# Kernel tuning notes

Hardware: AMD Instinct MI355X
Metric: run time of the kernel (lower is better)

The kernel has to match this reference:

```python
import jax, jax.numpy as jnp
import numpy as np

N, E, D, H, OUT, L, G = 50000, 800000, 128, 128, 128, 5, 512
EMB = L * H  # 640
BN_EPS = 1e-5


def setup_inputs() -> dict:
    key = jax.random.key(0)
    ks = jax.random.split(key, 24)
    s_h = 1.0 / np.sqrt(H)
    s_e = 1.0 / np.sqrt(EMB)
    inp = {
        'x': jax.random.normal(ks[0], (N, D), jnp.float32),
        'edge_index': jax.random.randint(ks[1], (2, E), 0, N, jnp.int32),
        'batch': jnp.sort(jax.random.randint(ks[2], (N,), 0, G, jnp.int32)),
        # per-layer GINConv MLP: Linear(D/H->H), BN(H), ReLU, Linear(H->H). D==H so stackable.
        'conv_W1': jax.random.normal(ks[3], (L, H, H), jnp.float32) * s_h,
        'conv_b1': jnp.zeros((L, H), jnp.float32),
        'conv_g1': jnp.ones((L, H), jnp.float32),
        'conv_be1': jnp.zeros((L, H), jnp.float32),
        'conv_W2': jax.random.normal(ks[4], (L, H, H), jnp.float32) * s_h,
        'conv_b2': jnp.zeros((L, H), jnp.float32),
        'eps': jnp.zeros((L,), jnp.float32),  # train_eps=True, init 0.0
        # outer BatchNorm per layer
        'bn_g': jnp.ones((L, H), jnp.float32),
        'bn_b': jnp.zeros((L, H), jnp.float32),
        # per-layer prediction heads Linear(H -> OUT)
        'pred_W': jax.random.normal(ks[5], (L, H, OUT), jnp.float32) * s_h,
        'pred_b': jnp.zeros((L, OUT), jnp.float32),
        # global_d FF(EMB): 3 stacked Linear(EMB,EMB) + shortcut
        'gW': jax.random.normal(ks[6], (3, EMB, EMB), jnp.float32) * s_e,
        'gb': jnp.zeros((3, EMB), jnp.float32),
        'gsW': jax.random.normal(ks[7], (EMB, EMB), jnp.float32) * s_e,
        'gsb': jnp.zeros((EMB,), jnp.float32),
        # local_d FF(EMB)
        'lW': jax.random.normal(ks[8], (3, EMB, EMB), jnp.float32) * s_e,
        'lb': jnp.zeros((3, EMB), jnp.float32),
        'lsW': jax.random.normal(ks[9], (EMB, EMB), jnp.float32) * s_e,
        'lsb': jnp.zeros((EMB,), jnp.float32),
    }
    return inp


def _bn(h, g, b):
    # BatchNorm1d, training mode: batch stats over node dim (biased var)
    m = jnp.mean(h, axis=0)
    v = jnp.var(h, axis=0)
    return g * (h - m) * jax.lax.rsqrt(v + BN_EPS) + b


def _ff(x, W, b, Ws, bs):
    h = x
    for i in range(3):
        h = jax.nn.relu(h @ W[i] + b[i])
    return h + x @ Ws + bs


def reference(x, edge_index, batch, conv_W1, conv_b1, conv_g1, conv_be1,
              conv_W2, conv_b2, eps, bn_g, bn_b, pred_W, pred_b,
              gW, gb, gsW, gsb, lW, lb, lsW, lsb):
    src, dst = edge_index[0], edge_index[1]
    h = x
    xs = []
    for i in range(L):
        # GINConv: (1+eps)*x_i + sum_{j->i} x_j, then MLP
        agg = jax.ops.segment_sum(h[src], dst, num_segments=N)
        h = (1.0 + eps[i]) * h + agg
        h = _bn(h @ conv_W1[i] + conv_b1[i], conv_g1[i], conv_be1[i])
        h = jax.nn.relu(h)
        h = h @ conv_W2[i] + conv_b2[i]
        h = jax.nn.relu(_bn(h, bn_g[i], bn_b[i]))
        xs.append(h)
    # per-layer graph sum-pool + prediction head (dropout in eval = identity)
    xpool = [jax.ops.segment_sum(xs[i], batch, num_segments=G) @ pred_W[i] + pred_b[i]
             for i in range(L)]
    xcat = jnp.concatenate(xpool, axis=1)            # [G, L*OUT]
    graph_embedding = _ff(xcat, gW, gb, gsW, gsb)     # [G, EMB]
    node_embedding = _ff(jnp.concatenate(xs, axis=1), lW, lb, lsW, lsb)  # [N, EMB]
    return (graph_embedding, node_embedding, xcat)
```

## Files before the change

### kernel.cpp

```cpp
#include <hip/hip_runtime.h>

constexpr int H    = 128;
constexpr int LNUM = 5;
constexpr int NG   = 512;
constexpr int EMB  = 640;
constexpr float BN_EPS = 1e-5f;

typedef __attribute__((ext_vector_type(8))) short bf16x8;
typedef __attribute__((ext_vector_type(4))) float f32x4;

__device__ inline unsigned short f2bf(float f){
  unsigned u = __builtin_bit_cast(unsigned, f);
  u += 0x7FFF + ((u >> 16) & 1);
  return (unsigned short)(u >> 16);
}
__device__ inline float bf2f(unsigned short h){
  unsigned u = ((unsigned)h) << 16;
  return __builtin_bit_cast(float, u);
}

__device__ inline int xcd_swz(int bid, int nwg){
  int q = nwg >> 3, r = nwg & 7;
  int xcd = bid & 7, idx = bid >> 3;
  return (xcd < r ? xcd*(q+1) : r*(q+1) + (xcd-r)*q) + idx;
}

__global__ void k_zerof(float* p, int n){
  int i = blockIdx.x*256 + threadIdx.x;
  if (i < n) p[i] = 0.f;
}
__global__ void k_zeroi(int* p, int n){
  int i = blockIdx.x*256 + threadIdx.x;
  if (i < n) p[i] = 0;
}

__global__ void k_hist(const int* __restrict__ dst, int E, int* deg){
  int e = blockIdx.x*256 + threadIdx.x;
  if (e < E) atomicAdd(&deg[dst[e]], 1);
}

__global__ __launch_bounds__(1024) void k_scan(int* degcur, int* __restrict__ rowptr, int n){
  __shared__ int wsum[16];
  __shared__ int carry;
  int tid = threadIdx.x, wid = tid >> 6, lane = tid & 63;
  if (tid == 0){ carry = 0; rowptr[0] = 0; }
  __syncthreads();
  for (int base = 0; base < n; base += 1024){
    int v = (base + tid < n) ? degcur[base + tid] : 0;
    int s = v;
#pragma unroll
    for (int off = 1; off < 64; off <<= 1){
      int t = __shfl_up(s, off);
      if (lane >= off) s += t;
    }
    if (lane == 63) wsum[wid] = s;
    __syncthreads();
    if (wid == 0 && lane < 16){
      int wv = wsum[lane];
#pragma unroll
      for (int off = 1; off < 16; off <<= 1){
        int t = __shfl_up(wv, off);
        if (lane >= off) wv += t;
      }
      wsum[lane] = wv;
    }
    __syncthreads();
    int incl = s + (wid ? wsum[wid-1] : 0) + carry;
    if (base + tid < n){ rowptr[base + tid + 1] = incl; degcur[base + tid] = incl - v; }
    __syncthreads();
    if (tid == 0) carry += wsum[15];
    __syncthreads();
  }
}

__global__ void k_scatter(const int* __restrict__ src, const int* __restrict__ dst,
                          int E, int* cursor, int* __restrict__ colsrc){
  int e = blockIdx.x*256 + threadIdx.x;
  if (e < E){
    int d = dst[e];
    int pos = atomicAdd(&cursor[d], 1);
    colsrc[pos] = src[e];
  }
}

__global__ void k_gstart(const int* __restrict__ batch, int N, int* __restrict__ gstart){
  int g = blockIdx.x*256 + threadIdx.x;
  if (g <= NG){
    int lo = 0, hi = N;
    while (lo < hi){
      int mid = (lo + hi) >> 1;
      if (batch[mid] < g) lo = mid + 1; else hi = mid;
    }
    gstart[g] = lo;
  }
}

__global__ void k_castT(const float* __restrict__ W, unsigned short* __restrict__ Wt,
                        int K, int Nn, int ldt, int koff){
  __shared__ float sh[32][33];
  const size_t in_off  = (size_t)blockIdx.z * K * Nn;
  const size_t out_off = (size_t)blockIdx.z * Nn * ldt;
  int n0 = blockIdx.x*32, k0 = blockIdx.y*32;
  int tx = threadIdx.x, ty = threadIdx.y;
  for (int r = ty; r < 32; r += 8)
    sh[r][tx] = W[in_off + (size_t)(k0 + r)*Nn + n0 + tx];
  __syncthreads();
  for (int r = ty; r < 32; r += 8)
    Wt[out_off + (size_t)(n0 + r)*ldt + koff + k0 + tx] = f2bf(sh[tx][r]);
}

__global__ void k_bias2(const float* __restrict__ a, const float* __restrict__ b,
                        float* __restrict__ o){
  int i = threadIdx.x;
  o[i] = a[i] + b[i];
}

template<bool IN_BF16>
__global__ __launch_bounds__(256) void k_agg(const void* __restrict__ hin_, int ldh,
                                             const int* __restrict__ rowptr,
                                             const int* __restrict__ colsrc,
                                             const float* __restrict__ epsp,
                                             unsigned short* __restrict__ outp, int nN){
  int node = blockIdx.x*4 + (threadIdx.x >> 6);
  if (node >= nN) return;
  int lane = threadIdx.x & 63;
  float a0, a1;
  if (IN_BF16){
    unsigned u = ((const unsigned*)hin_)[((size_t)node*ldh >> 1) + lane];
    a0 = bf2f((unsigned short)u); a1 = bf2f((unsigned short)(u >> 16));
  } else {
    float2 f = ((const float2*)hin_)[((size_t)node*ldh >> 1) + lane];
    a0 = f.x; a1 = f.y;
  }
  float ep = 1.0f + *epsp;
  a0 *= ep; a1 *= ep;
  int e = rowptr[node], e1 = rowptr[node+1];
  const int ld2 = ldh >> 1;
  for (; e + 4 <= e1; e += 4){
    int s0 = colsrc[e], s1 = colsrc[e+1], s2 = colsrc[e+2], s3 = colsrc[e+3];
    if (IN_BF16){
      unsigned u0 = ((const unsigned*)hin_)[(size_t)s0*ld2 + lane];
      unsigned u1 = ((const unsigned*)hin_)[(size_t)s1*ld2 + lane];
      unsigned u2 = ((const unsigned*)hin_)[(size_t)s2*ld2 + lane];
      unsigned u3 = ((const unsigned*)hin_)[(size_t)s3*ld2 + lane];
      a0 += bf2f((unsigned short)u0) + bf2f((unsigned short)u1)
          + bf2f((unsigned short)u2) + bf2f((unsigned short)u3);
      a1 += bf2f((unsigned short)(u0 >> 16)) + bf2f((unsigned short)(u1 >> 16))
          + bf2f((unsigned short)(u2 >> 16)) + bf2f((unsigned short)(u3 >> 16));
    } else {
      float2 f0 = ((const float2*)hin_)[(size_t)s0*ld2 + lane];
      float2 f1 = ((const float2*)hin_)[(size_t)s1*ld2 + lane];
      float2 f2 = ((const float2*)hin_)[(size_t)s2*ld2 + lane];
      float2 f3 = ((const float2*)hin_)[(size_t)s3*ld2 + lane];
      a0 += f0.x + f1.x + f2.x + f3.x;
      a1 += f0.y + f1.y + f2.y + f3.y;
    }
  }
  for (; e < e1; ++e){
    int s = colsrc[e];
    if (IN_BF16){
      unsigned u = ((const unsigned*)hin_)[(size_t)s*ld2 + lane];
      a0 += bf2f((unsigned short)u); a1 += bf2f((unsigned short)(u >> 16));
    } else {
      float2 f = ((const float2*)hin_)[(size_t)s*ld2 + lane];
      a0 += f.x; a1 += f.y;
    }
  }
  ((unsigned*)outp)[((size_t)node*H >> 1) + lane] =
      (unsigned)f2bf(a0) | ((unsigned)f2bf(a1) << 16);
}

__global__ void k_bnfin(float* sums, float* sumsq,
                        const float* __restrict__ g, const float* __restrict__ b,
                        float* __restrict__ scale, float* __restrict__ shift, float invn){
  int c = threadIdx.x;
  float m = sums[c]*invn;
  float v = sumsq[c]*invn - m*m;
  float inv = rsqrtf(v + BN_EPS);
  float sc = g[c]*inv;
  scale[c] = sc;
  shift[c] = b[c] - m*sc;
  sums[c] = 0.f; sumsq[c] = 0.f;
}

__global__ __launch_bounds__(256) void k_bnapply(const unsigned short* __restrict__ U,
                                                 const float* __restrict__ scale,
                                                 const float* __restrict__ shift,
                                                 unsigned short* __restrict__ out,
                                                 int ldo, int n){
  int i = blockIdx.x*256 + threadIdx.x;
  int total = n * (H/4);
  if (i < total){
    int r = i >> 5;
    int c4 = (i & 31) << 2;
    uint2 up = *(const uint2*)(U + (size_t)r*H + c4);
    float4 sc = *(const float4*)(scale + c4);
    float4 sf = *(const float4*)(shift + c4);
    float a = fmaxf(fmaf(sc.x, bf2f((unsigned short)up.x),        sf.x), 0.f);
    float b = fmaxf(fmaf(sc.y, bf2f((unsigned short)(up.x>>16)),  sf.y), 0.f);
    float c = fmaxf(fmaf(sc.z, bf2f((unsigned short)up.y),        sf.z), 0.f);
    float d = fmaxf(fmaf(sc.w, bf2f((unsigned short)(up.y>>16)),  sf.w), 0.f);
    uint2 o;
    o.x = (unsigned)f2bf(a) | ((unsigned)f2bf(b) << 16);
    o.y = (unsigned)f2bf(c) | ((unsigned)f2bf(d) << 16);
    *(uint2*)(out + (size_t)r*ldo + c4) = o;
  }
}

__global__ __launch_bounds__(320) void k_pool(const unsigned short* __restrict__ xall,
                                              const int* __restrict__ gstart,
                                              float* __restrict__ pooled){
  int g = blockIdx.x;
  int t = threadIdx.x;
  int n0 = gstart[g], n1 = gstart[g+1];
  float a0 = 0.f, a1 = 0.f;
  for (int n = n0; n < n1; ++n){
    unsigned u = ((const unsigned*)xall)[(size_t)n*(EMB/2) + t];
    a0 += bf2f((unsigned short)u); a1 += bf2f((unsigned short)(u >> 16));
  }
  *(float2*)(pooled + (size_t)g*EMB + 2*t) = make_float2(a0, a1);
}

__global__ __launch_bounds__(128) void k_pred(const float* __restrict__ pooled,
                                              const float* __restrict__ W,
                                              const float* __restrict__ b,
                                              float* __restrict__ xcat){
  int g = blockIdx.x, l = blockIdx.y, o = threadIdx.x;
  __shared__ float sh[128];
  sh[o] = pooled[(size_t)g*EMB + l*H + o];
  __syncthreads();
  const float* Wl = W + (size_t)l*H*H;
  float acc = b[l*H + o];
  for (int k = 0; k < H; ++k) acc = fmaf(sh[k], Wl[k*H + o], acc);
  xcat[(size_t)g*EMB + l*H + o] = acc;
}

template<bool RELU, bool OUT_BF16, bool DUAL>
__global__ __launch_bounds__(512) void k_mm(
    const unsigned short* __restrict__ A, int lda,
    const unsigned short* __restrict__ A2,
    const unsigned short* __restrict__ Bt, int ldb,
    const float* __restrict__ bias,
    void* __restrict__ Cv, int ldc,
    int M, int K)
{
  __shared__ union LdsU {
    unsigned short stage[2][2][128*64];
    unsigned short sc16[128*136];
    float          sc32[128*132];
  } u;
  const int tid  = threadIdx.x;
  const int lane = tid & 63;
  const int w    = tid >> 6;
  const int wr   = w >> 2, wc = w & 3;

  const int nwg = gridDim.x * gridDim.y;
  const int bid = blockIdx.y * gridDim.x + blockIdx.x;
  const int wg  = xcd_swz(bid, nwg);
  const int col0 = (wg % gridDim.x) * 128;
  const int row0 = (wg / gridDim.x) * 128;
  const int KA   = DUAL ? (K >> 1) : K;

  const unsigned short *sA[2], *sA2[2], *sB[2];
  int dOff[2];
#pragma unroll
  for (int j = 0; j < 2; ++j){
    int d = w*2048 + j*1024 + lane*16;
    int m = d >> 7;
    int inner = (d & 127) ^ ((m & 7) << 4);
    int gm = row0 + m; if (gm > M-1) gm = M-1;
    sA[j]  = A  + (size_t)gm*lda + (inner >> 1);
    if (DUAL) sA2[j] = A2 + (size_t)gm*lda + (inner >> 1);
    sB[j]  = Bt + (size_t)(col0 + m)*ldb + (inner >> 1);
    dOff[j] = w*2048 + j*1024;
  }

  f32x4 acc[4][2];
#pragma unroll
  for (int i = 0; i < 4; ++i)
#pragma unroll
    for (int j = 0; j < 2; ++j)
      acc[i][j] = (f32x4){0.f, 0.f, 0.f, 0.f};

  auto STAGE = [&](int buf, int kt){
    int k0 = kt*64;
    int ka = k0;
    bool second = DUAL && (k0 >= KA);
    if (second) ka = k0 - KA;
#pragma unroll
    for (int j = 0; j < 2; ++j){
      const unsigned short* srcA = second ? (sA2[j] + ka) : (sA[j] + ka);
      __builtin_amdgcn_global_load_lds(
          (const __attribute__((address_space(1))) void*)srcA,
          (__attribute__((address_space(3))) void*)((char*)&u.stage[buf][0][0] + dOff[j]),
          16, 0, 0);
    }
#pragma unroll
    for (int j = 0; j < 2; ++j)
      __builtin_amdgcn_global_load_lds(
          (const __attribute__((address_space(1))) void*)(sB[j] + k0),
          (__attribute__((address_space(3))) void*)((char*)&u.stage[buf][1][0] + dOff[j]),
          16, 0, 0);
  };

  auto COMPUTE = [&](int buf){
    const char* Ab = (const char*)&u.stage[buf][0][0];
    const char* Bb = (const char*)&u.stage[buf][1][0];
#pragma unroll
    for (int kk = 0; kk < 2; ++kk){
      const int kb = kk*64 + ((lane >> 4) << 4);
      bf16x8 af[4], bfr[2];
#pragma unroll
      for (int i = 0; i < 4; ++i){
        int row = wr*64 + i*16 + (lane & 15);
        int ab  = (row*128 + kb) ^ ((row & 7) << 4);
        af[i] = *(const bf16x8*)(Ab + ab);
      }
#pragma unroll
      for (int j = 0; j < 2; ++j){
        int col = wc*32 + j*16 + (lane & 15);
        int bb  = (col*128 + kb) ^ ((col & 7) << 4);
        bfr[j] = *(const bf16x8*)(Bb + bb);
      }
#pragma unroll
      for (int i = 0; i < 4; ++i)
#pragma unroll
        for (int j = 0; j < 2; ++j)
          acc[i][j] = __builtin_amdgcn_mfma_f32_16x16x32_bf16(af[i], bfr[j], acc[i][j], 0, 0, 0);
    }
  };

  const int NT = K / 64;
  STAGE(0, 0);
  STAGE(1, 1);
  asm volatile("s_waitcnt vmcnt(4)" ::: "memory");
  __syncthreads();

  int cur = 0;
  for (int t = 0; t < NT; ++t){
    COMPUTE(cur);
    if (t == NT-1) break;
    __syncthreads();
    if (t + 2 < NT){
      STAGE(cur, t + 2);
      asm volatile("s_waitcnt vmcnt(4)" ::: "memory");
    } else {
      asm volatile("s_waitcnt vmcnt(0)" ::: "memory");
    }
    __syncthreads();
    cur ^= 1;
  }

  __syncthreads();
  if (OUT_BF16){
#pragma unroll
    for (int j = 0; j < 2; ++j){
      int cl = wc*32 + j*16 + (lane & 15);
      float bs = bias[col0 + cl];
#pragma unroll
      for (int i = 0; i < 4; ++i){
        int rb = wr*64 + i*16 + ((lane >> 4) << 2);
#pragma unroll
        for (int r = 0; r < 4; ++r){
          float v = acc[i][j][r] + bs;
          if (RELU) v = fmaxf(v, 0.f);
          u.sc16[(rb + r)*136 + cl] = f2bf(v);
        }
      }
    }
    __syncthreads();
    unsigned short* Cb = (unsigned short*)Cv;
    for (int idx = tid; idx < 128*16; idx += 512){
      int rr = idx >> 4, seg = idx & 15;
      int grow = row0 + rr;
      if (grow < M){
        uint4 vv = *(const uint4*)&u.sc16[rr*136 + seg*8];
        *(uint4*)(Cb + (size_t)grow*ldc + col0 + seg*8) = vv;
      }
    }
  } else {
#pragma unroll
    for (int j = 0; j < 2; ++j){
      int cl = wc*32 + j*16 + (lane & 15);
      float bs = bias[col0 + cl];
#pragma unroll
      for (int i = 0; i < 4; ++i){
        int rb = wr*64 + i*16 + ((lane >> 4) << 2);
#pragma unroll
        for (int r = 0; r < 4; ++r){
          float v = acc[i][j][r] + bs;
          if (RELU) v = fmaxf(v, 0.f);
          u.sc32[(rb + r)*132 + cl] = v;
        }
      }
    }
    __syncthreads();
    float* Cf = (float*)Cv;
    for (int idx = tid; idx < 128*32; idx += 512){
      int rr = idx >> 5, seg = idx & 31;
      int grow = row0 + rr;
      if (grow < M){
        float4 vv = *(const float4*)&u.sc32[rr*132 + seg*4];
        *(float4*)(Cf + (size_t)grow*ldc + col0 + seg*4) = vv;
      }
    }
  }
}

template<bool PRO_BN, bool STATS>
__global__ __launch_bounds__(512) void k_mmc(
    const unsigned short* __restrict__ A,
    const unsigned short* __restrict__ Bt,
    const float* __restrict__ bias,
    const float* __restrict__ kscale, const float* __restrict__ kshift,
    unsigned short* __restrict__ C, int ldc,
    float* sums, float* sumsq,
    int M)
{
  __shared__ unsigned short shm[2*128*128];
  unsigned short* As = shm;
  unsigned short* Bs = shm + 128*128;
  const int tid  = threadIdx.x;
  const int lane = tid & 63;
  const int w    = tid >> 6;
  const int wr   = w >> 2, wc = w & 3;

  const int wg   = xcd_swz(blockIdx.x, gridDim.x);
  const int row0 = wg * 128;

#pragma unroll
  for (int j = 0; j < 4; ++j){
    int d = w*4096 + j*1024 + lane*16;
    int m = d >> 8;
    int inner = (d & 255) ^ ((m & 15) << 4);
    int gm = row0 + m; if (gm > M-1) gm = M-1;
    __builtin_amdgcn_global_load_lds(
        (const __attribute__((address_space(1))) void*)(A + (size_t)gm*H + (inner >> 1)),
        (__attribute__((address_space(3))) void*)((char*)As + w*4096 + j*1024),
        16, 0, 0);
    __builtin_amdgcn_global_load_lds(
        (const __attribute__((address_space(1))) void*)(Bt + (size_t)m*H + (inner >> 1)),
        (__attribute__((address_space(3))) void*)((char*)Bs + w*4096 + j*1024),
        16, 0, 0);
  }
  asm volatile("s_waitcnt vmcnt(0)" ::: "memory");
  __syncthreads();

  f32x4 acc[4][2];
#pragma unroll
  for (int i = 0; i < 4; ++i)
#pragma unroll
    for (int j = 0; j < 2; ++j)
      acc[i][j] = (f32x4){0.f, 0.f, 0.f, 0.f};

#pragma unroll
  for (int kk = 0; kk < 4; ++kk){
    const int kb = kk*64 + ((lane >> 4) << 4);
    bf16x8 af[4], bfr[2];
#pragma unroll
    for (int i = 0; i < 4; ++i){
      int row = wr*64 + i*16 + (lane & 15);
      int ab  = (row*256 + kb) ^ ((row & 15) << 4);
      af[i] = *(const bf16x8*)((const char*)As + ab);
    }
#pragma unroll
    for (int j = 0; j < 2; ++j){
      int col = wc*32 + j*16 + (lane & 15);
      int bb  = (col*256 + kb) ^ ((col & 15) << 4);
      bfr[j] = *(const bf16x8*)((const char*)Bs + bb);
    }
    if (PRO_BN){
      int k8 = kk*32 + ((lane >> 4) << 3);
      float4 s0 = *(const float4*)(kscale + k8), s1 = *(const float4*)(kscale + k8 + 4);
      float4 f0 = *(const float4*)(kshift + k8), f1 = *(const float4*)(kshift + k8 + 4);
      float sc[8] = {s0.x,s0.y,s0.z,s0.w,s1.x,s1.y,s1.z,s1.w};
      float sf[8] = {f0.x,f0.y,f0.z,f0.w,f1.x,f1.y,f1.z,f1.w};
#pragma unroll
      for (int i = 0; i < 4; ++i){
        bf16x8 a = af[i], o;
#pragma unroll
        for (int jj = 0; jj < 8; ++jj){
          float v = fmaxf(fmaf(sc[jj], bf2f((unsigned short)a[jj]), sf[jj]), 0.f);
          o[jj] = (short)f2bf(v);
        }
        af[i] = o;
      }
    }
#pragma unroll
    for (int i = 0; i < 4; ++i)
#pragma unroll
      for (int j = 0; j < 2; ++j)
        acc[i][j] = __builtin_amdgcn_mfma_f32_16x16x32_bf16(af[i], bfr[j], acc[i][j], 0, 0, 0);
  }

  if (STATS){
#pragma unroll
    for (int j = 0; j < 2; ++j){
      int col = wc*32 + j*16 + (lane & 15);
      float bs = bias[col];
      float s = 0.f, q = 0.f;
#pragma unroll
      for (int i = 0; i < 4; ++i){
        int rb = row0 + wr*64 + i*16 + ((lane >> 4) << 2);
#pragma unroll
        for (int r = 0; r < 4; ++r){
          if (rb + r < M){
            float v = acc[i][j][r] + bs;
            s += v; q += v*v;
          }
        }
      }
      s += __shfl_xor(s, 16); q += __shfl_xor(q, 16);
      s += __shfl_xor(s, 32); q += __shfl_xor(q, 32);
      if (lane < 16){
        atomicAdd(&sums[col], s);
        atomicAdd(&sumsq[col], q);
      }
    }
  }

  __syncthreads();
#pragma unroll
  for (int j = 0; j < 2; ++j){
    int cl = wc*32 + j*16 + (lane & 15);
    float bs = bias[cl];
#pragma unroll
    for (int i = 0; i < 4; ++i){
      int rb = wr*64 + i*16 + ((lane >> 4) << 2);
#pragma unroll
      for (int r = 0; r < 4; ++r)
        shm[(rb + r)*136 + cl] = f2bf(acc[i][j][r] + bs);
    }
  }
  __syncthreads();
  for (int idx = tid; idx < 128*16; idx += 512){
    int rr = idx >> 4, seg = idx & 15;
    int grow = row0 + rr;
    if (grow < M){
      uint4 vv = *(const uint4*)&shm[rr*136 + seg*8];
      *(uint4*)(C + (size_t)grow*ldc + seg*8) = vv;
    }
  }
}

template<bool RELU, bool ADD_D>
__global__ __launch_bounds__(256) void k_gemm64(
    const float* __restrict__ A, int lda,
    const float* __restrict__ B, int ldb,
    const float* __restrict__ bias,
    const float* D, int ldd,
    float* C, int ldc,
    int M, int N, int K)
{
  __shared__ float As[32][68];
  __shared__ float Bs[32][64];
  const int tid  = threadIdx.x;
  const int tx   = tid & 15;
  const int ty   = tid >> 4;
  const int row0 = blockIdx.x * 64;
  const int col0 = blockIdx.y * 64;
  const int am = tid >> 3;
  const int ak = (tid & 7) << 2;
  const int bk = tid >> 4;
  const int bn = (tid & 15) << 2;
  float acc[4][4] = {};

  for (int k0 = 0; k0 < K; k0 += 32){
#pragma unroll
    for (int h = 0; h < 2; ++h){
      int m  = am + h*32;
      int gr = row0 + m;
      float4 v = make_float4(0.f, 0.f, 0.f, 0.f);
      if (gr < M) v = *(const float4*)(A + (size_t)gr*lda + k0 + ak);
      As[ak+0][m]=v.x; As[ak+1][m]=v.y; As[ak+2][m]=v.z; As[ak+3][m]=v.w;
    }
#pragma unroll
    for (int h = 0; h < 2; ++h){
      int kk = bk + h*16;
      *(float4*)(&Bs[kk][bn]) = *(const float4*)(B + (size_t)(k0+kk)*ldb + col0 + bn);
    }
    __syncthreads();
#pragma unroll 8
    for (int k = 0; k < 32; ++k){
      float4 a = *(const float4*)(&As[k][ty<<2]);
      float4 b = *(const float4*)(&Bs[k][tx<<2]);
      float av[4] = {a.x,a.y,a.z,a.w};
      float bv[4] = {b.x,b.y,b.z,b.w};
#pragma unroll
      for (int i = 0; i < 4; ++i)
#pragma unroll
        for (int j = 0; j < 4; ++j)
          acc[i][j] = fmaf(av[i], bv[j], acc[i][j]);
    }
    __syncthreads();
  }

  const int col = col0 + (tx<<2);
  float4 bv = *(const float4*)(bias + col);
#pragma unroll
  for (int i = 0; i < 4; ++i){
    int row = row0 + (ty<<2) + i;
    if (row < M){
      float r[4] = {acc[i][0]+bv.x, acc[i][1]+bv.y, acc[i][2]+bv.z, acc[i][3]+bv.w};
      if (RELU){
#pragma unroll
        for (int j = 0; j < 4; ++j) r[j] = fmaxf(r[j], 0.f);
      }
      if (ADD_D){
        float4 d = *(const float4*)(D + (size_t)row*ldd + col);
        r[0]+=d.x; r[1]+=d.y; r[2]+=d.z; r[3]+=d.w;
      }
      *(float4*)(C + (size_t)row*ldc + col) = make_float4(r[0],r[1],r[2],r[3]);
    }
  }
}

extern "C" void kernel_launch(void* const* d_in, const int* in_sizes, int n_in,
                              void* d_out, int out_size, void* d_ws, size_t ws_size,
                              hipStream_t stream) {
  const float* x        = (const float*)d_in[0];
  const int*   ei       = (const int*)d_in[1];
  const int*   batch    = (const int*)d_in[2];
  const float* conv_W1  = (const float*)d_in[3];
  const float* conv_b1  = (const float*)d_in[4];
  const float* conv_g1  = (const float*)d_in[5];
  const float* conv_be1 = (const float*)d_in[6];
  const float* conv_W2  = (const float*)d_in[7];
  const float* conv_b2  = (const float*)d_in[8];
  const float* epsv     = (const float*)d_in[9];
  const float* bn_g     = (const float*)d_in[10];
  const float* bn_b     = (const float*)d_in[11];
  const float* pred_W   = (const float*)d_in[12];
  const float* pred_b   = (const float*)d_in[13];
  const float* gW       = (const float*)d_in[14];
  const float* gb       = (const float*)d_in[15];
  const float* gsW      = (const float*)d_in[16];
  const float* gsb      = (const float*)d_in[17];
  const float* lW       = (const float*)d_in[18];
  const float* lb       = (const float*)d_in[19];
  const float* lsW      = (const float*)d_in[20];
  const float* lsb      = (const float*)d_in[21];

  const int N = in_sizes[0] / H;
  const int E = in_sizes[1] / 2;
  const int* srcI = ei;
  const int* dstI = ei + E;

  float* out = (float*)d_out;
  float* GE = out;
  float* NE = out + (size_t)NG*EMB;
  float* XC = NE + (size_t)N*EMB;

  unsigned short* xall = (unsigned short*)d_ws;
  unsigned short* h1   = xall + (size_t)N*EMB;
  unsigned short* h2   = h1 + (size_t)N*EMB;
  unsigned short* hpre = h1;
  unsigned short* ub   = h1 + (size_t)N*H;
  unsigned short* tb   = h1 + (size_t)2*N*H;

  float* pooled  = (float*)(h2 + (size_t)N*EMB);
  float* gtmp1   = pooled + (size_t)NG*EMB;
  float* gtmp2   = gtmp1 + (size_t)NG*EMB;
  float* sums    = gtmp2 + (size_t)NG*EMB;
  float* sumsq   = sums + 128;
  float* bnscale = sumsq + 128;
  float* bnshift = bnscale + 128;
  float* biasNE  = bnshift + 128;
  unsigned short* W1t   = (unsigned short*)(biasNE + EMB);
  unsigned short* W2t   = W1t + (size_t)LNUM*H*H;
  unsigned short* lWt01 = W2t + (size_t)LNUM*H*H;
  unsigned short* Wcat  = lWt01 + (size_t)2*EMB*EMB;
  int* rowptr = (int*)(Wcat + (size_t)2*EMB*EMB);
  int* cursor = rowptr + (N + 1);
  int* colsrc = cursor + N;
  int* gstart = colsrc + E;

  k_zerof<<<1, 256, 0, stream>>>(sums, 256);

  k_zeroi<<<(N+255)/256, 256, 0, stream>>>(cursor, N);
  k_hist<<<(E+255)/256, 256, 0, stream>>>(dstI, E, cursor);
  k_scan<<<1, 1024, 0, stream>>>(cursor, rowptr, N);
  k_scatter<<<(E+255)/256, 256, 0, stream>>>(srcI, dstI, E, cursor, colsrc);
  k_gstart<<<(NG+256)/256, 256, 0, stream>>>(batch, N, gstart);

  const dim3 tb32(32, 8);
  k_castT<<<dim3(H/32, H/32, LNUM), tb32, 0, stream>>>(conv_W1, W1t, H, H, H, 0);
  k_castT<<<dim3(H/32, H/32, LNUM), tb32, 0, stream>>>(conv_W2, W2t, H, H, H, 0);
  k_castT<<<dim3(EMB/32, EMB/32, 2), tb32, 0, stream>>>(lW, lWt01, EMB, EMB, EMB, 0);
  k_castT<<<dim3(EMB/32, EMB/32, 1), tb32, 0, stream>>>(lW + (size_t)2*EMB*EMB, Wcat,
                                                        EMB, EMB, 2*EMB, 0);
  k_castT<<<dim3(EMB/32, EMB/32, 1), tb32, 0, stream>>>(lsW, Wcat, EMB, EMB, 2*EMB, EMB);
  k_bias2<<<1, EMB, 0, stream>>>(lb + (size_t)2*EMB, lsb, biasNE);

  const float invn = 1.0f / (float)N;
  const int nrow = (N + 127)/128;

  for (int l = 0; l < LNUM; ++l){
    if (l == 0)
      k_agg<false><<<(N+3)/4, 256, 0, stream>>>(x, H, rowptr, colsrc, epsv, hpre, N);
    else
      k_agg<true><<<(N+3)/4, 256, 0, stream>>>(xall + (size_t)(l-1)*H, EMB, rowptr, colsrc,
                                               epsv + l, hpre, N);

    k_mmc<false,true><<<nrow, 512, 0, stream>>>(
        hpre, W1t + (size_t)l*H*H, conv_b1 + l*H, nullptr, nullptr,
        ub, H, sums, sumsq, N);
    k_bnfin<<<1, 128, 0, stream>>>(sums, sumsq, conv_g1 + l*H, conv_be1 + l*H,
                                   bnscale, bnshift, invn);
    k_mmc<true,true><<<nrow, 512, 0, stream>>>(
        ub, W2t + (size_t)l*H*H, conv_b2 + l*H, bnscale, bnshift,
        tb, H, sums, sumsq, N);
    k_bnfin<<<1, 128, 0, stream>>>(sums, sumsq, bn_g + l*H, bn_b + l*H,
                                   bnscale, bnshift, invn);
    k_bnapply<<<(N*32 + 255)/256, 256, 0, stream>>>(tb, bnscale, bnshift,
                                                    xall + (size_t)l*H, EMB, N);
  }

  k_pool<<<NG, 320, 0, stream>>>(xall, gstart, pooled);
  k_pred<<<dim3(NG, LNUM), 128, 0, stream>>>(pooled, pred_W, pred_b, XC);

  const dim3 gg((NG + 63)/64, EMB/64);
  k_gemm64<false,false><<<gg, 256, 0, stream>>>(XC, EMB, gsW, EMB, gsb,
                                                nullptr, 0, GE, EMB, NG, EMB, EMB);
  k_gemm64<true,false><<<gg, 256, 0, stream>>>(XC, EMB, gW, EMB, gb,
                                               nullptr, 0, gtmp1, EMB, NG, EMB, EMB);
  k_gemm64<true,false><<<gg, 256, 0, stream>>>(gtmp1, EMB, gW + (size_t)EMB*EMB, EMB, gb + EMB,
                                               nullptr, 0, gtmp2, EMB, NG, EMB, EMB);
  k_gemm64<true,true><<<gg, 256, 0, stream>>>(gtmp2, EMB, gW + (size_t)2*EMB*EMB, EMB, gb + 2*EMB,
                                              GE, EMB, GE, EMB, NG, EMB, EMB);

  const dim3 gn(EMB/128, nrow);
  k_mm<true,true,false><<<gn, 512, 0, stream>>>(
      xall, EMB, nullptr, lWt01, EMB, lb, h1, EMB, N, EMB);
  k_mm<true,true,false><<<gn, 512, 0, stream>>>(
      h1, EMB, nullptr, lWt01 + (size_t)EMB*EMB, EMB, lb + EMB, h2, EMB, N, EMB);
  k_mm<false,false,true><<<gn, 512, 0, stream>>>(
      h2, EMB, xall, Wcat, 2*EMB, biasNE, NE, EMB, N, 2*EMB);
}
```

Measured before the change: 1.181 ms.

## Enlarge node-FF GEMM tile to 256x128 with triple-buffered LDS staging

The k_mm GEMM used for the three node-embedding feed-forward layers now computes 256x128 output tiles per 512-thread block instead of 128x128. Each wave handles a 64x64 sub-tile with 16 MFMA accumulators, which raises arithmetic intensity per LDS load and halves how often B is re-read. The staging pipeline moves from two to three LDS buffers, issuing the next load before compute so there is one barrier per k-step instead of two. The fp32 epilogue writes its output in two halves to fit the shared-memory union. The cost is more LDS per block (144 KB for staging) and more accumulator registers, which lowers occupancy, and a coarser grid of about 196x5 blocks.

New measurement: 1.195 ms. No clear change (+1.2%).

```diff
diff --git a/kernel.cpp b/kernel.cpp
--- a/kernel.cpp
+++ b/kernel.cpp
@@ -245,87 +245,92 @@
     int M, int K)
 {
   __shared__ union LdsU {
-    unsigned short stage[2][2][128*64];
-    unsigned short sc16[128*136];
+    unsigned short stage[3][24576];
+    unsigned short sc16[256*136];
     float          sc32[128*132];
   } u;
   const int tid  = threadIdx.x;
   const int lane = tid & 63;
   const int w    = tid >> 6;
-  const int wr   = w >> 2, wc = w & 3;
+  const int wr   = w >> 1, wc = w & 1;
 
   const int nwg = gridDim.x * gridDim.y;
   const int bid = blockIdx.y * gridDim.x + blockIdx.x;
   const int wg  = xcd_swz(bid, nwg);
   const int col0 = (wg % gridDim.x) * 128;
-  const int row0 = (wg / gridDim.x) * 128;
+  const int row0 = (wg / gridDim.x) * 256;
   const int KA   = DUAL ? (K >> 1) : K;
 
-  const unsigned short *sA[2], *sA2[2], *sB[2];
-  int dOff[2];
+  const unsigned short *sA[4], *sA2[4], *sB[2];
+  int dA[4], dB[2];
+#pragma unroll
+  for (int j = 0; j < 4; ++j){
+    int d = w*4096 + j*1024 + lane*16;
+    int m = d >> 7;
+    int inner = (d & 127) ^ ((m & 7) << 4);
+    int gm = row0 + m; if (gm > M-1) gm = M-1;
+    sA[j] = A + (size_t)gm*lda + (inner >> 1);
+    if (DUAL) sA2[j] = A2 + (size_t)gm*lda + (inner >> 1);
+    dA[j] = w*4096 + j*1024;
+  }
 #pragma unroll
   for (int j = 0; j < 2; ++j){
     int d = w*2048 + j*1024 + lane*16;
     int m = d >> 7;
     int inner = (d & 127) ^ ((m & 7) << 4);
-    int gm = row0 + m; if (gm > M-1) gm = M-1;
-    sA[j]  = A  + (size_t)gm*lda + (inner >> 1);
-    if (DUAL) sA2[j] = A2 + (size_t)gm*lda + (inner >> 1);
-    sB[j]  = Bt + (size_t)(col0 + m)*ldb + (inner >> 1);
-    dOff[j] = w*2048 + j*1024;
-  }
-
-  f32x4 acc[4][2];
+    sB[j] = Bt + (size_t)(col0 + m)*ldb + (inner >> 1);
+    dB[j] = 32768 + w*2048 + j*1024;
+  }
+
+  f32x4 acc[4][4];
 #pragma unroll
   for (int i = 0; i < 4; ++i)
 #pragma unroll
-    for (int j = 0; j < 2; ++j)
+    for (int j = 0; j < 4; ++j)
       acc[i][j] = (f32x4){0.f, 0.f, 0.f, 0.f};
 
   auto STAGE = [&](int buf, int kt){
-    int k0 = kt*64;
-    int ka = k0;
+    int k0 = kt*64, ka = k0;
     bool second = DUAL && (k0 >= KA);
     if (second) ka = k0 - KA;
-#pragma unroll
-    for (int j = 0; j < 2; ++j){
-      const unsigned short* srcA = second ? (sA2[j] + ka) : (sA[j] + ka);
+    char* base = (char*)&u.stage[buf][0];
+#pragma unroll
+    for (int j = 0; j < 4; ++j){
+      const unsigned short* s = second ? (sA2[j] + ka) : (sA[j] + ka);
       __builtin_amdgcn_global_load_lds(
-          (const __attribute__((address_space(1))) void*)srcA,
-          (__attribute__((address_space(3))) void*)((char*)&u.stage[buf][0][0] + dOff[j]),
+          (const __attribute__((address_space(1))) void*)s,
+          (__attribute__((address_space(3))) void*)(base + dA[j]),
           16, 0, 0);
     }
 #pragma unroll
     for (int j = 0; j < 2; ++j)
       __builtin_amdgcn_global_load_lds(
           (const __attribute__((address_space(1))) void*)(sB[j] + k0),
-          (__attribute__((address_space(3))) void*)((char*)&u.stage[buf][1][0] + dOff[j]),
+          (__attribute__((address_space(3))) void*)(base + dB[j]),
           16, 0, 0);
   };
 
   auto COMPUTE = [&](int buf){
-    const char* Ab = (const char*)&u.stage[buf][0][0];
-    const char* Bb = (const char*)&u.stage[buf][1][0];
+    const char* Ab = (const char*)&u.stage[buf][0];
+    const char* Bb = Ab + 32768;
 #pragma unroll
     for (int kk = 0; kk < 2; ++kk){
       const int kb = kk*64 + ((lane >> 4) << 4);
-      bf16x8 af[4], bfr[2];
+      bf16x8 af[4], bfr[4];
 #pragma unroll
       for (int i = 0; i < 4; ++i){
         int row = wr*64 + i*16 + (lane & 15);
-        int ab  = (row*128 + kb) ^ ((row & 7) << 4);
-        af[i] = *(const bf16x8*)(Ab + ab);
-      }
-#pragma unroll
-      for (int j = 0; j < 2; ++j){
-        int col = wc*32 + j*16 + (lane & 15);
-        int bb  = (col*128 + kb) ^ ((col & 7) << 4);
-        bfr[j] = *(const bf16x8*)(Bb + bb);
+        af[i] = *(const bf16x8*)(Ab + ((row*128 + kb) ^ ((row & 7) << 4)));
+      }
+#pragma unroll
+      for (int j = 0; j < 4; ++j){
+        int col = wc*64 + j*16 + (lane & 15);
+        bfr[j] = *(const bf16x8*)(Bb + ((col*128 + kb) ^ ((col & 7) << 4)));
       }
 #pragma unroll
       for (int i = 0; i < 4; ++i)
 #pragma unroll
-        for (int j = 0; j < 2; ++j)
+        for (int j = 0; j < 4; ++j)
           acc[i][j] = __builtin_amdgcn_mfma_f32_16x16x32_bf16(af[i], bfr[j], acc[i][j], 0, 0, 0);
     }
   };
@@ -333,29 +338,26 @@
   const int NT = K / 64;
   STAGE(0, 0);
   STAGE(1, 1);
-  asm volatile("s_waitcnt vmcnt(4)" ::: "memory");
+  asm volatile("s_waitcnt vmcnt(6)" ::: "memory");
   __syncthreads();
 
-  int cur = 0;
   for (int t = 0; t < NT; ++t){
-    COMPUTE(cur);
-    if (t == NT-1) break;
-    __syncthreads();
-    if (t + 2 < NT){
-      STAGE(cur, t + 2);
-      asm volatile("s_waitcnt vmcnt(4)" ::: "memory");
-    } else {
-      asm volatile("s_waitcnt vmcnt(0)" ::: "memory");
-    }
-    __syncthreads();
-    cur ^= 1;
+    if (t + 2 < NT) STAGE((t + 2) % 3, t + 2);
+    COMPUTE(t % 3);
+    if (t < NT - 1){
+      if (t + 2 < NT)
+        asm volatile("s_waitcnt vmcnt(6)" ::: "memory");
+      else
+        asm volatile("s_waitcnt vmcnt(0)" ::: "memory");
+      __syncthreads();
+    }
   }
 
   __syncthreads();
   if (OUT_BF16){
 #pragma unroll
-    for (int j = 0; j < 2; ++j){
-      int cl = wc*32 + j*16 + (lane & 15);
+    for (int j = 0; j < 4; ++j){
+      int cl = wc*64 + j*16 + (lane & 15);
       float bs = bias[col0 + cl];
 #pragma unroll
       for (int i = 0; i < 4; ++i){
@@ -370,7 +372,7 @@
     }
     __syncthreads();
     unsigned short* Cb = (unsigned short*)Cv;
-    for (int idx = tid; idx < 128*16; idx += 512){
+    for (int idx = tid; idx < 256*16; idx += 512){
       int rr = idx >> 4, seg = idx & 15;
       int grow = row0 + rr;
       if (grow < M){
@@ -379,30 +381,36 @@
       }
     }
   } else {
-#pragma unroll
-    for (int j = 0; j < 2; ++j){
-      int cl = wc*32 + j*16 + (lane & 15);
-      float bs = bias[col0 + cl];
-#pragma unroll
-      for (int i = 0; i < 4; ++i){
-        int rb = wr*64 + i*16 + ((lane >> 4) << 2);
-#pragma unroll
-        for (int r = 0; r < 4; ++r){
-          float v = acc[i][j][r] + bs;
-          if (RELU) v = fmaxf(v, 0.f);
-          u.sc32[(rb + r)*132 + cl] = v;
+    float* Cf = (float*)Cv;
+#pragma unroll
+    for (int p = 0; p < 2; ++p){
+      if ((wr >> 1) == p){
+#pragma unroll
+        for (int j = 0; j < 4; ++j){
+          int cl = wc*64 + j*16 + (lane & 15);
+          float bs = bias[col0 + cl];
+#pragma unroll
+          for (int i = 0; i < 4; ++i){
+            int lr = (wr & 1)*64 + i*16 + ((lane >> 4) << 2);
+#pragma unroll
+            for (int r = 0; r < 4; ++r){
+              float v = acc[i][j][r] + bs;
+              if (RELU) v = fmaxf(v, 0.f);
+              u.sc32[(lr + r)*132 + cl] = v;
+            }
+          }
         }
       }
-    }
-    __syncthreads();
-    float* Cf = (float*)Cv;
-    for (int idx = tid; idx < 128*32; idx += 512){
-      int rr = idx >> 5, seg = idx & 31;
-      int grow = row0 + rr;
-      if (grow < M){
-        float4 vv = *(const float4*)&u.sc32[rr*132 + seg*4];
-        *(float4*)(Cf + (size_t)grow*ldc + col0 + seg*4) = vv;
-      }
+      __syncthreads();
+      for (int idx = tid; idx < 128*32; idx += 512){
+        int rr = idx >> 5, seg = idx & 31;
+        int grow = row0 + p*128 + rr;
+        if (grow < M){
+          float4 vv = *(const float4*)&u.sc32[rr*132 + seg*4];
+          *(float4*)(Cf + (size_t)grow*ldc + col0 + seg*4) = vv;
+        }
+      }
+      __syncthreads();
     }
   }
 }
@@ -729,7 +737,8 @@
   k_gemm64<true,true><<<gg, 256, 0, stream>>>(gtmp2, EMB, gW + (size_t)2*EMB*EMB, EMB, gb + 2*EMB,
                                               GE, EMB, GE, EMB, NG, EMB, EMB);
 
-  const dim3 gn(EMB/128, nrow);
+  const int nrow256 = (N + 255)/256;
+  const dim3 gn(EMB/128, nrow256);
   k_mm<true,true,false><<<gn, 512, 0, stream>>>(
       xall, EMB, nullptr, lWt01, EMB, lb, h1, EMB, N, EMB);
   k_mm<true,true,false><<<gn, 512, 0, stream>>>(
```
